# Kernel optimization log

Hardware: AMD Instinct MI355X
Metric: run time of the kernel (lower is better)

The kernel has to match this reference:

```python
import jax, jax.numpy as jnp
import numpy as np

EMBED_DIM = 384
NUM_HEADS = 6
HEAD_DIM = EMBED_DIM // NUM_HEADS
SCALE = HEAD_DIM ** (-0.5)


def setup_inputs() -> dict:
    key = jax.random.key(0)
    ks = jax.random.split(key, 5)
    B, N, D = 8, 2048, EMBED_DIM
    x = jax.random.normal(ks[0], (B, N, D), dtype=jnp.float32)
    # Linear params, torch convention: weight [out, in], bias [out]
    w_qkv = jax.random.normal(ks[1], (3 * D, D), dtype=jnp.float32) * (D ** -0.5)
    b_qkv = jax.random.normal(ks[2], (3 * D,), dtype=jnp.float32) * 0.01
    w_out = jax.random.normal(ks[3], (D, D), dtype=jnp.float32) * (D ** -0.5)
    b_out = jax.random.normal(ks[4], (D,), dtype=jnp.float32) * 0.01
    return {"x": x, "w_qkv": w_qkv, "b_qkv": b_qkv, "w_out": w_out, "b_out": b_out}


def reference(x, w_qkv, b_qkv, w_out, b_out):
    B, N, D = x.shape
    H, Dh = NUM_HEADS, HEAD_DIM
    # qkv projection: [B,N,3D]
    qkv = jnp.einsum('bnd,ed->bne', x, w_qkv) + b_qkv
    qkv = qkv.reshape(B, N, 3, H, Dh).transpose(2, 0, 3, 1, 4)  # [3,B,H,N,Dh]
    q, k, v = qkv[0], qkv[1], qkv[2]
    # full NxN attention scores (faithful to original eager math)
    scores = jnp.einsum('bhnd,bhmd->bhnm', q, k) * SCALE  # [B,H,N,N]
    attn = jax.nn.softmax(scores, axis=-1)
    out = jnp.einsum('bhnm,bhmd->bhnd', attn, v)  # [B,H,N,Dh]
    out = out.transpose(0, 2, 1, 3).reshape(B, N, D)
    out = jnp.einsum('bnd,ed->bne', out, w_out) + b_out
    return out
```

## Files before the change

### kernel.cpp

```cpp
#include <hip/hip_runtime.h>

typedef unsigned short u16;
typedef unsigned int u32;
typedef float f32x4 __attribute__((ext_vector_type(4)));
typedef __bf16 bf16x8 __attribute__((ext_vector_type(8)));
typedef unsigned short u16x8 __attribute__((ext_vector_type(8)));
typedef unsigned short u16x4 __attribute__((ext_vector_type(4)));
typedef unsigned int u32x4 __attribute__((ext_vector_type(4)));

__device__ inline u16 f2bf(float f) {
    return __builtin_bit_cast(u16, (__bf16)f);
}

__device__ inline void gll16(const u16* g, u16* l) {
    u16* gnc = const_cast<u16*>(g);
    __builtin_amdgcn_global_load_lds((__attribute__((address_space(1))) u32*)gnc,
                                     (__attribute__((address_space(3))) u32*)l,
                                     16, 0, 0);
}

#define MFMA(a, b, c) __builtin_amdgcn_mfma_f32_16x16x32_bf16((a), (b), (c), 0, 0, 0)

#define C_SHIFT 17.3123405f
#define Q_SCALE 0.1803368801f

__global__ __launch_bounds__(256)
void cvt_kernel(const float* __restrict__ X, const float* __restrict__ Wq,
                const float* __restrict__ Wo, u16* __restrict__ Xb,
                u16* __restrict__ Wqb, u16* __restrict__ Wob)
{
    int i = blockIdx.x * 256 + threadIdx.x;
    const float* src; u16* dst; int off;
    if (i < 1572864)       { src = X;  dst = Xb;  off = i; }
    else if (i < 1683456)  { src = Wq; dst = Wqb; off = i - 1572864; }
    else                   { src = Wo; dst = Wob; off = i - 1683456; }
    f32x4 v = *(const f32x4*)&src[off * 4];
    u16x4 p;
    for (int k = 0; k < 4; ++k) p[k] = f2bf(v[k]);
    *(u16x4*)&dst[off * 4] = p;
}

__global__ __launch_bounds__(256)
void qkv_kernel(const u16* __restrict__ Xb, const u16* __restrict__ Wqb,
                const float* __restrict__ B, u16* __restrict__ Qo,
                u16* __restrict__ Ko, u16* __restrict__ VTo)
{
    __shared__ __align__(128) u16 As[128][64];
    __shared__ __align__(128) u16 Ws[128][64];
    const int tid = threadIdx.x;
    const int m0 = blockIdx.x * 128;
    const int n0 = blockIdx.y * 128;
    const int wv = tid >> 6, lane = tid & 63;
    const int l15 = lane & 15, quad = lane >> 4;
    const int mw = (wv & 1) * 64, nw = (wv >> 1) * 64;

    const int lr = lane >> 3;
    const int gsrc = (lane & 7) ^ lr;
    const int swz = (quad ^ (l15 & 7)) * 8;

    f32x4 acc[4][4] = {};
    for (int kt = 0; kt < 384; kt += 64) {
        __syncthreads();
#pragma unroll
        for (int i = 0; i < 4; ++i) {
            int r = (wv * 4 + i) * 8 + lr;
            gll16(&Xb[(m0 + r) * 384 + kt + gsrc * 8], &As[(wv * 4 + i) * 8][0]);
            gll16(&Wqb[(n0 + r) * 384 + kt + gsrc * 8], &Ws[(wv * 4 + i) * 8][0]);
        }
        __syncthreads();
#pragma unroll
        for (int kc = 0; kc < 2; ++kc) {
            bf16x8 a[4], bf[4];
#pragma unroll
            for (int mi = 0; mi < 4; ++mi)
                a[mi] = *(const bf16x8*)&As[mw + mi * 16 + l15][swz ^ (kc << 5)];
#pragma unroll
            for (int nj = 0; nj < 4; ++nj)
                bf[nj] = *(const bf16x8*)&Ws[nw + nj * 16 + l15][swz ^ (kc << 5)];
#pragma unroll
            for (int mi = 0; mi < 4; ++mi)
#pragma unroll
                for (int nj = 0; nj < 4; ++nj)
                    acc[mi][nj] = MFMA(bf[nj], a[mi], acc[mi][nj]);
        }
    }
#pragma unroll
    for (int nj = 0; nj < 4; ++nj) {
        const int colb = n0 + nw + nj * 16 + quad * 4;
        const int t = colb / 384;
        const int hd = (colb % 384) / 64;
        const int dh0 = colb & 63;
        const f32x4 bv = *(const f32x4*)&B[colb];
#pragma unroll
        for (int mi = 0; mi < 4; ++mi) {
            const int gm = m0 + mw + mi * 16 + l15;
            const int bb = gm >> 11, n = gm & 2047;
            const int bh = bb * 6 + hd;
            if (t == 0) {
                u16x4 p;
#pragma unroll
                for (int r = 0; r < 4; ++r)
                    p[r] = f2bf((acc[mi][nj][r] + bv[r]) * Q_SCALE);
                *(u16x4*)&Qo[(bh * 2048 + n) * 64 + dh0] = p;
            } else if (t == 1) {
                u16x4 p;
#pragma unroll
                for (int r = 0; r < 4; ++r)
                    p[r] = f2bf(acc[mi][nj][r] + bv[r]);
                *(u16x4*)&Ko[(bh * 2048 + n) * 64 + dh0] = p;
            } else {
                const int nn = (n & ~31) | (((n >> 2) & 3) << 3)
                             | (((n >> 4) & 1) << 2) | (n & 3);
#pragma unroll
                for (int r = 0; r < 4; ++r)
                    VTo[(bh * 64 + dh0 + r) * 2048 + nn] =
                        f2bf(acc[mi][nj][r] + bv[r]);
            }
        }
    }
}

__global__ __launch_bounds__(512)
void attn_kernel(const u16* __restrict__ Q, const u16* __restrict__ K,
                 const u16* __restrict__ VT, u16* __restrict__ O)
{
    __shared__ __align__(128) u16 Ks[2][64][64];
    __shared__ __align__(128) u16 VTs[2][64][64];
    __shared__ __align__(16) float lbuf[128];

    const int tid = threadIdx.x;
    const int lin = blockIdx.y * 16 + blockIdx.x;
    const int lin2 = (lin & 7) * 96 + (lin >> 3);
    const int bh = lin2 >> 4;
    const int q0 = (lin2 & 15) * 128;
    const int wv = tid >> 6, lane = tid & 63;
    const int l15 = lane & 15, quad = lane >> 4;
    const int qsub = wv & 3, kh = wv >> 2;

    bf16x8 qf[2][2];
#pragma unroll
    for (int qb = 0; qb < 2; ++qb) {
        const u16* qptr = &Q[(bh * 2048 + q0 + qsub * 32 + qb * 16 + l15) * 64 + quad * 8];
        qf[qb][0] = *(const bf16x8*)qptr;
        qf[qb][1] = *(const bf16x8*)(qptr + 32);
    }

    const int lr = lane >> 3;
    const int gsrc = (lane & 7) ^ lr;
    const u16* ksrc = &K[(bh * 2048 + wv * 8 + lr) * 64 + gsrc * 8];
    const u16* vsrc = &VT[(bh * 64 + wv * 8 + lr) * 2048 + gsrc * 8];
    const int swz = (quad ^ (l15 & 7)) * 8;

    const f32x4 cinit = {-C_SHIFT, -C_SHIFT, -C_SHIFT, -C_SHIFT};
    float l_part[2] = {};
    f32x4 acc[2][4] = {};

    gll16(ksrc, &Ks[0][wv * 8][0]);
    gll16(vsrc, &VTs[0][wv * 8][0]);

    for (int j = 0; j < 32; ++j) {
        const int cur = j & 1;
        __syncthreads();
        if (j < 31) {
            gll16(ksrc + (j + 1) * 4096, &Ks[cur ^ 1][wv * 8][0]);
            gll16(vsrc + (j + 1) * 64, &VTs[cur ^ 1][wv * 8][0]);
        }

        u32 w[2][2][2];
#pragma unroll
        for (int c = 0; c < 2; ++c) {
            const u16* krow = &Ks[cur][kh * 32 + c * 16 + l15][0];
            bf16x8 a0 = *(const bf16x8*)(krow + swz);
            bf16x8 a1 = *(const bf16x8*)(krow + (swz ^ 32));
#pragma unroll
            for (int qb = 0; qb < 2; ++qb) {
                f32x4 s = MFMA(a0, qf[qb][0], cinit);
                s = MFMA(a1, qf[qb][1], s);
                float p0 = __builtin_amdgcn_exp2f(s[0]);
                float p1 = __builtin_amdgcn_exp2f(s[1]);
                float p2 = __builtin_amdgcn_exp2f(s[2]);
                float p3 = __builtin_amdgcn_exp2f(s[3]);
                l_part[qb] += p0;
                l_part[qb] += p1;
                l_part[qb] += p2;
                l_part[qb] += p3;
                w[qb][c][0] = (u32)f2bf(p0) | ((u32)f2bf(p1) << 16);
                w[qb][c][1] = (u32)f2bf(p2) | ((u32)f2bf(p3) << 16);
            }
        }

        bf16x8 pf[2];
#pragma unroll
        for (int qb = 0; qb < 2; ++qb) {
            u32x4 t = {w[qb][0][0], w[qb][0][1], w[qb][1][0], w[qb][1][1]};
            pf[qb] = __builtin_bit_cast(bf16x8, t);
        }

#pragma unroll
        for (int ct = 0; ct < 4; ++ct) {
            bf16x8 bv = *(const bf16x8*)(&VTs[cur][ct * 16 + l15][0] + (swz ^ (kh << 5)));
#pragma unroll
            for (int qb = 0; qb < 2; ++qb)
                acc[qb][ct] = MFMA(pf[qb], bv, acc[qb][ct]);
        }
    }

    float lh[2];
#pragma unroll
    for (int qb = 0; qb < 2; ++qb) {
        float t = l_part[qb];
        t += __shfl_xor(t, 16);
        t += __shfl_xor(t, 32);
        lh[qb] = t;
    }
    __syncthreads();
    if (kh == 1) {
        float* sb = (qsub < 2) ? (float*)&Ks[qsub][0][0] : (float*)&VTs[qsub - 2][0][0];
#pragma unroll
        for (int qb = 0; qb < 2; ++qb)
#pragma unroll
            for (int ct = 0; ct < 4; ++ct)
                *(f32x4*)&sb[((qb * 4 + ct) * 64 + lane) * 4] = acc[qb][ct];
        if (quad == 0) {
            lbuf[qsub * 32 + l15] = lh[0];
            lbuf[qsub * 32 + 16 + l15] = lh[1];
        }
    }
    __syncthreads();
    if (kh == 0) {
        float* sb = (qsub < 2) ? (float*)&Ks[qsub][0][0] : (float*)&VTs[qsub - 2][0][0];
#pragma unroll
        for (int qb = 0; qb < 2; ++qb)
#pragma unroll
            for (int ct = 0; ct < 4; ++ct)
                acc[qb][ct] += *(const f32x4*)&sb[((qb * 4 + ct) * 64 + lane) * 4];
        lh[0] += lbuf[qsub * 32 + l15];
        lh[1] += lbuf[qsub * 32 + 16 + l15];
        int b = bh / 6, h = bh % 6;
#pragma unroll
        for (int qb = 0; qb < 2; ++qb) {
            float li[4];
            for (int r = 0; r < 4; ++r) li[r] = 1.0f / __shfl(lh[qb], quad * 4 + r);
            for (int ct = 0; ct < 4; ++ct)
                for (int r = 0; r < 4; ++r) {
                    int row = q0 + qsub * 32 + qb * 16 + quad * 4 + r;
                    int dh = ct * 16 + l15;
                    O[(b * 2048 + row) * 384 + h * 64 + dh] = f2bf(acc[qb][ct][r] * li[r]);
                }
        }
    }
}

__global__ __launch_bounds__(256)
void outproj_kernel(const u16* __restrict__ A, const u16* __restrict__ Wob,
                    const float* __restrict__ B, float* __restrict__ out)
{
    __shared__ __align__(16) u16 As[64][72];
    __shared__ __align__(16) u16 Ws[64][72];
    const int tid = threadIdx.x;
    const int m0 = blockIdx.x * 64;
    const int n0 = blockIdx.y * 64;
    const int wv = tid >> 6, lane = tid & 63;
    const int l15 = lane & 15, quad = lane >> 4;

    f32x4 acc[4] = {};
    for (int kt = 0; kt < 384; kt += 64) {
        __syncthreads();
        for (int c = tid; c < 512; c += 256) {
            int row = c >> 3, cc = (c & 7) * 8;
            *(u16x8*)&As[row][cc] = *(const u16x8*)&A[(m0 + row) * 384 + kt + cc];
            *(u16x8*)&Ws[row][cc] = *(const u16x8*)&Wob[(n0 + row) * 384 + kt + cc];
        }
        __syncthreads();
        for (int kc = 0; kc < 2; ++kc) {
            bf16x8 b = *(const bf16x8*)&Ws[wv * 16 + l15][kc * 32 + quad * 8];
            for (int mi = 0; mi < 4; ++mi) {
                bf16x8 a = *(const bf16x8*)&As[mi * 16 + l15][kc * 32 + quad * 8];
                acc[mi] = MFMA(a, b, acc[mi]);
            }
        }
    }
    const int col = n0 + wv * 16 + l15;
    const float bias = B[col];
    for (int mi = 0; mi < 4; ++mi)
        for (int r = 0; r < 4; ++r) {
            int gm = m0 + mi * 16 + quad * 4 + r;
            out[gm * 384 + col] = acc[mi][r] + bias;
        }
}

extern "C" void kernel_launch(void* const* d_in, const int* in_sizes, int n_in,
                              void* d_out, int out_size, void* d_ws, size_t ws_size,
                              hipStream_t stream) {
    const float* x     = (const float*)d_in[0];
    const float* w_qkv = (const float*)d_in[1];
    const float* b_qkv = (const float*)d_in[2];
    const float* w_out = (const float*)d_in[3];
    const float* b_out = (const float*)d_in[4];
    float* out = (float*)d_out;

    char* ws = (char*)d_ws;
    u16* Qw   = (u16*)(ws);
    u16* Kw   = (u16*)(ws + 12582912);
    u16* VTw  = (u16*)(ws + 25165824);
    u16* XbAw = (u16*)(ws + 37748736);
    u16* Wqb  = (u16*)(ws + 50331648);
    u16* Wob  = (u16*)(ws + 51216384);

    cvt_kernel<<<6720, 256, 0, stream>>>(x, w_qkv, w_out, XbAw, Wqb, Wob);
    qkv_kernel<<<dim3(128, 9), 256, 0, stream>>>(XbAw, Wqb, b_qkv, Qw, Kw, VTw);
    attn_kernel<<<dim3(16, 48), 512, 0, stream>>>(Qw, Kw, VTw, XbAw);
    outproj_kernel<<<dim3(256, 6), 256, 0, stream>>>(XbAw, Wob, b_out, out);
}
```

Before: 197.5 us.

## Load GEMM operands directly from global into registers, drop LDS staging

The QKV and output-projection GEMMs now read MFMA operand fragments straight from global memory (relying on L1/L2) and no longer stage tiles through shared memory with barriers. The output projection is also retiled to 128x64 blocks with 4x2 MFMA tiles per wave and vectorised float4 stores. This removes the LDS round trips and syncthreads, but the reads are strided per lane and less coalesced, and operands are re-read by each wave instead of being shared through LDS.

```diff
diff --git a/kernel.cpp b/kernel.cpp
--- a/kernel.cpp
+++ b/kernel.cpp
@@ -45,8 +45,6 @@
                 const float* __restrict__ B, u16* __restrict__ Qo,
                 u16* __restrict__ Ko, u16* __restrict__ VTo)
 {
-    __shared__ __align__(128) u16 As[128][64];
-    __shared__ __align__(128) u16 Ws[128][64];
     const int tid = threadIdx.x;
     const int m0 = blockIdx.x * 128;
     const int n0 = blockIdx.y * 128;
@@ -54,35 +52,25 @@
     const int l15 = lane & 15, quad = lane >> 4;
     const int mw = (wv & 1) * 64, nw = (wv >> 1) * 64;
 
-    const int lr = lane >> 3;
-    const int gsrc = (lane & 7) ^ lr;
-    const int swz = (quad ^ (l15 & 7)) * 8;
+    const u16* xb = &Xb[(m0 + mw + l15) * 384 + quad * 8];
+    const u16* wb = &Wqb[(n0 + nw + l15) * 384 + quad * 8];
 
     f32x4 acc[4][4] = {};
-    for (int kt = 0; kt < 384; kt += 64) {
-        __syncthreads();
-#pragma unroll
-        for (int i = 0; i < 4; ++i) {
-            int r = (wv * 4 + i) * 8 + lr;
-            gll16(&Xb[(m0 + r) * 384 + kt + gsrc * 8], &As[(wv * 4 + i) * 8][0]);
-            gll16(&Wqb[(n0 + r) * 384 + kt + gsrc * 8], &Ws[(wv * 4 + i) * 8][0]);
-        }
-        __syncthreads();
-#pragma unroll
-        for (int kc = 0; kc < 2; ++kc) {
-            bf16x8 a[4], bf[4];
-#pragma unroll
-            for (int mi = 0; mi < 4; ++mi)
-                a[mi] = *(const bf16x8*)&As[mw + mi * 16 + l15][swz ^ (kc << 5)];
+#pragma unroll
+    for (int ks = 0; ks < 12; ++ks) {
+        const int ko = ks * 32;
+        bf16x8 a[4], bf[4];
+#pragma unroll
+        for (int mi = 0; mi < 4; ++mi)
+            a[mi] = *(const bf16x8*)(xb + mi * 16 * 384 + ko);
+#pragma unroll
+        for (int nj = 0; nj < 4; ++nj)
+            bf[nj] = *(const bf16x8*)(wb + nj * 16 * 384 + ko);
+#pragma unroll
+        for (int mi = 0; mi < 4; ++mi)
 #pragma unroll
             for (int nj = 0; nj < 4; ++nj)
-                bf[nj] = *(const bf16x8*)&Ws[nw + nj * 16 + l15][swz ^ (kc << 5)];
-#pragma unroll
-            for (int mi = 0; mi < 4; ++mi)
-#pragma unroll
-                for (int nj = 0; nj < 4; ++nj)
-                    acc[mi][nj] = MFMA(bf[nj], a[mi], acc[mi][nj]);
-        }
+                acc[mi][nj] = MFMA(bf[nj], a[mi], acc[mi][nj]);
     }
 #pragma unroll
     for (int nj = 0; nj < 4; ++nj) {
@@ -255,38 +243,46 @@
 void outproj_kernel(const u16* __restrict__ A, const u16* __restrict__ Wob,
                     const float* __restrict__ B, float* __restrict__ out)
 {
-    __shared__ __align__(16) u16 As[64][72];
-    __shared__ __align__(16) u16 Ws[64][72];
     const int tid = threadIdx.x;
-    const int m0 = blockIdx.x * 64;
+    const int m0 = blockIdx.x * 128;
     const int n0 = blockIdx.y * 64;
     const int wv = tid >> 6, lane = tid & 63;
     const int l15 = lane & 15, quad = lane >> 4;
-
-    f32x4 acc[4] = {};
-    for (int kt = 0; kt < 384; kt += 64) {
-        __syncthreads();
-        for (int c = tid; c < 512; c += 256) {
-            int row = c >> 3, cc = (c & 7) * 8;
-            *(u16x8*)&As[row][cc] = *(const u16x8*)&A[(m0 + row) * 384 + kt + cc];
-            *(u16x8*)&Ws[row][cc] = *(const u16x8*)&Wob[(n0 + row) * 384 + kt + cc];
-        }
-        __syncthreads();
-        for (int kc = 0; kc < 2; ++kc) {
-            bf16x8 b = *(const bf16x8*)&Ws[wv * 16 + l15][kc * 32 + quad * 8];
-            for (int mi = 0; mi < 4; ++mi) {
-                bf16x8 a = *(const bf16x8*)&As[mi * 16 + l15][kc * 32 + quad * 8];
-                acc[mi] = MFMA(a, b, acc[mi]);
-            }
-        }
-    }
-    const int col = n0 + wv * 16 + l15;
-    const float bias = B[col];
-    for (int mi = 0; mi < 4; ++mi)
-        for (int r = 0; r < 4; ++r) {
-            int gm = m0 + mi * 16 + quad * 4 + r;
-            out[gm * 384 + col] = acc[mi][r] + bias;
-        }
+    const int mw = (wv & 1) * 64, nw = (wv >> 1) * 32;
+
+    const u16* ab = &A[(m0 + mw + l15) * 384 + quad * 8];
+    const u16* wb = &Wob[(n0 + nw + l15) * 384 + quad * 8];
+
+    f32x4 acc[4][2] = {};
+#pragma unroll
+    for (int ks = 0; ks < 12; ++ks) {
+        const int ko = ks * 32;
+        bf16x8 a[4], bf[2];
+#pragma unroll
+        for (int mi = 0; mi < 4; ++mi)
+            a[mi] = *(const bf16x8*)(ab + mi * 16 * 384 + ko);
+#pragma unroll
+        for (int nj = 0; nj < 2; ++nj)
+            bf[nj] = *(const bf16x8*)(wb + nj * 16 * 384 + ko);
+#pragma unroll
+        for (int mi = 0; mi < 4; ++mi)
+#pragma unroll
+            for (int nj = 0; nj < 2; ++nj)
+                acc[mi][nj] = MFMA(bf[nj], a[mi], acc[mi][nj]);
+    }
+#pragma unroll
+    for (int nj = 0; nj < 2; ++nj) {
+        const int colb = n0 + nw + nj * 16 + quad * 4;
+        const f32x4 bv = *(const f32x4*)&B[colb];
+#pragma unroll
+        for (int mi = 0; mi < 4; ++mi) {
+            const int gm = m0 + mw + mi * 16 + l15;
+            f32x4 o = acc[mi][nj];
+#pragma unroll
+            for (int r = 0; r < 4; ++r) o[r] += bv[r];
+            *(f32x4*)&out[gm * 384 + colb] = o;
+        }
+    }
 }
 
 extern "C" void kernel_launch(void* const* d_in, const int* in_sizes, int n_in,
@@ -310,5 +306,5 @@
     cvt_kernel<<<6720, 256, 0, stream>>>(x, w_qkv, w_out, XbAw, Wqb, Wob);
     qkv_kernel<<<dim3(128, 9), 256, 0, stream>>>(XbAw, Wqb, b_qkv, Qw, Kw, VTw);
     attn_kernel<<<dim3(16, 48), 512, 0, stream>>>(Qw, Kw, VTw, XbAw);
-    outproj_kernel<<<dim3(256, 6), 256, 0, stream>>>(XbAw, Wob, b_out, out);
-}
+    outproj_kernel<<<dim3(128, 6), 256, 0, stream>>>(XbAw, Wob, b_out, out);
+}
```

Result: slower. 237.6 us (+20.3%).
